# Performance work log

Measured on AMD Instinct MI355X. Metric: run time of the kernel, lower is better.

The kernel has to match this reference:

```python
import jax, jax.numpy as jnp
import numpy as np

N_NODES = 50000
N_EDGES = 800000
D = 64
NEG_SLOPE = 0.01  # torch F.leaky_relu default


def _gin_layer(h, src, dst, eps, W, b, activate):
    # max-aggregate neighbor features: for each dst node, max over incoming src feats
    msg = h[src]  # [E, D] gather
    agg = jax.ops.segment_max(msg, dst, num_segments=N_NODES)  # [N, D]
    # DGL fills nodes with no in-edges with 0 for max reduce
    agg = jnp.where(jnp.isfinite(agg), agg, jnp.zeros((), h.dtype))
    out = ((1.0 + eps) * h + agg) @ W + b
    if activate:
        out = jnp.where(out >= 0, out, NEG_SLOPE * out)
    return out


def setup_inputs() -> dict:
    key = jax.random.key(0)
    ks = jax.random.split(key, 6)
    scale = 1.0 / np.sqrt(D)
    return {
        "n_feat": jax.random.normal(ks[0], (N_NODES, D), dtype=jnp.float32),
        "W0": jax.random.normal(ks[1], (D, D), dtype=jnp.float32) * scale,
        "b0": jnp.zeros((D,), jnp.float32),
        "W1": jax.random.normal(ks[2], (D, D), dtype=jnp.float32) * scale,
        "b1": jnp.zeros((D,), jnp.float32),
        "W2": jax.random.normal(ks[3], (D, D), dtype=jnp.float32) * scale,
        "b2": jnp.zeros((D,), jnp.float32),
        "eps": jnp.zeros((3,), jnp.float32),
        "src": jax.random.randint(ks[4], (N_EDGES,), 0, N_NODES, dtype=jnp.int32),
        "dst": jax.random.randint(ks[5], (N_EDGES,), 0, N_NODES, dtype=jnp.int32),
    }


def reference(n_feat, W0, b0, W1, b1, W2, b2, eps, src, dst):
    h = _gin_layer(n_feat, src, dst, eps[0], W0, b0, activate=True)
    h = _gin_layer(h, src, dst, eps[1], W1, b1, activate=True)
    h = _gin_layer(h, src, dst, eps[2], W2, b2, activate=False)  # last_activate=False
    return h
```

## Files before the change

kernel.cpp:

```cpp
#include <hip/hip_runtime.h>

#define N_NODES 50000
#define N_EDGES 800000
#define D 64
#define CAP 64
#define XLD 72

typedef short short8 __attribute__((ext_vector_type(8)));
typedef float floatx4 __attribute__((ext_vector_type(4)));

__device__ __forceinline__ unsigned short f32_to_bf16(float f) {
    unsigned int u = __float_as_uint(f);
    u += 0x7FFFu + ((u >> 16) & 1u);
    return (unsigned short)(u >> 16);
}
__device__ __forceinline__ float bf16_to_f32(unsigned short h) {
    return __uint_as_float((unsigned int)h << 16);
}

__global__ void __launch_bounds__(256) cvt_kernel(const float* __restrict__ in,
                                                  unsigned short* __restrict__ hb0,
                                                  unsigned short* __restrict__ hb1) {
    int t = blockIdx.x * 256 + threadIdx.x;
    float4 v = ((const float4*)in)[t];
    uint2 o;
    o.x = ((unsigned)f32_to_bf16(v.y) << 16) | f32_to_bf16(v.x);
    o.y = ((unsigned)f32_to_bf16(v.w) << 16) | f32_to_bf16(v.z);
    ((uint2*)hb0)[t] = o;
    if (blockIdx.x == 0) {
        int l = threadIdx.x;
        if (l < 64) hb0[(size_t)N_NODES * 64 + l] = 0xFF80u;
        else if (l < 128) hb1[(size_t)N_NODES * 64 + (l - 64)] = 0xFF80u;
    }
}

__global__ void __launch_bounds__(256) wprep_kernel(const float* __restrict__ W0,
                                                    const float* __restrict__ W1,
                                                    const float* __restrict__ W2,
                                                    unsigned short* __restrict__ wt_all) {
    const float* Ws[3] = {W0, W1, W2};
    const float* W = Ws[blockIdx.x];
    unsigned short* o = wt_all + blockIdx.x * 4096;
    for (int idx = threadIdx.x; idx < 4096; idx += 256) {
        int k = idx >> 6, n = idx & 63;
        o[n * 64 + k] = f32_to_bf16(W[idx]);
    }
}

__global__ void __launch_bounds__(256) fill_kernel(const int* __restrict__ src,
                                                   const int* __restrict__ dst,
                                                   int* __restrict__ cnt,
                                                   int* __restrict__ bucket) {
    int e = blockIdx.x * 256 + threadIdx.x;
    int t = dst[e];
    int slot = atomicAdd(&cnt[t], 1);
    if (slot < CAP) bucket[t * CAP + slot] = src[e] << 6;
}

__global__ void __launch_bounds__(256) pad_kernel(const int* __restrict__ cnt,
                                                  int* __restrict__ bucket) {
    int t = blockIdx.x * 256 + threadIdx.x;
    if (t >= N_NODES) return;
    int c = min(cnt[t], CAP);
    int e4 = (c + 3) & ~3;
    for (int s = c; s < e4; ++s) bucket[t * CAP + s] = N_NODES * 64;
}

__global__ void __launch_bounds__(256) layer_kernel(
        const unsigned short* __restrict__ hin,
        const int* __restrict__ cnt,
        const int* __restrict__ bucket,
        const unsigned short* __restrict__ wt,
        const float* __restrict__ bias,
        const float* __restrict__ eps_arr,
        int layer, int activate, int last,
        unsigned short* __restrict__ out_bf,
        float* __restrict__ out_f32) {
    __shared__ unsigned short xs[16 * XLD];

    const int tid = threadIdx.x;
    const int lane = tid & 63;
    const int wv = tid >> 6;
    const float ev = 1.0f + eps_arr[layer];

    const int r0 = blockIdx.x * 16 + wv * 4;

    int bvec[4], c_true[4], c4[4];
    float self[4];
#pragma unroll
    for (int j = 0; j < 4; ++j) {
        int rr = r0 + j;
        bvec[j] = bucket[rr * CAP + lane];
        c_true[j] = min(cnt[rr], CAP);
        c4[j] = (c_true[j] + 3) & ~3;
        self[j] = bf16_to_f32(hin[rr * 64 + lane]);
    }
    int cmax = max(max(c4[0], c4[1]), max(c4[2], c4[3]));

    float m[4] = {-INFINITY, -INFINITY, -INFINITY, -INFINITY};
    for (int i = 0; i < cmax; i += 4) {
#pragma unroll
        for (int j = 0; j < 4; ++j) {
            if (i < c4[j]) {
                int s0 = __builtin_amdgcn_readlane(bvec[j], i);
                int s1 = __builtin_amdgcn_readlane(bvec[j], i + 1);
                int s2 = __builtin_amdgcn_readlane(bvec[j], i + 2);
                int s3 = __builtin_amdgcn_readlane(bvec[j], i + 3);
                float a0 = bf16_to_f32(hin[s0 + lane]);
                float a1 = bf16_to_f32(hin[s1 + lane]);
                float a2 = bf16_to_f32(hin[s2 + lane]);
                float a3 = bf16_to_f32(hin[s3 + lane]);
                m[j] = fmaxf(m[j], fmaxf(fmaxf(a0, a1), fmaxf(a2, a3)));
            }
        }
    }

#pragma unroll
    for (int j = 0; j < 4; ++j) {
        float agg = (c_true[j] > 0) ? m[j] : 0.0f;
        float x = fmaf(ev, self[j], agg);
        xs[(wv * 4 + j) * XLD + lane] = f32_to_bf16(x);
    }
    __syncthreads();

    const int l15 = lane & 15, hi = lane >> 4;
    const int kc = hi * 8;
    short8 a0 = *(const short8*)&xs[l15 * XLD + kc];
    short8 a1 = *(const short8*)&xs[l15 * XLD + 32 + kc];
    const int ncol = wv * 16 + l15;
    short8 b0 = *(const short8*)&wt[ncol * 64 + kc];
    short8 b1 = *(const short8*)&wt[ncol * 64 + 32 + kc];
    floatx4 acc = {0.f, 0.f, 0.f, 0.f};
    acc = __builtin_amdgcn_mfma_f32_16x16x32_bf16(a0, b0, acc, 0, 0, 0);
    acc = __builtin_amdgcn_mfma_f32_16x16x32_bf16(a1, b1, acc, 0, 0, 0);

    const float bv = bias[ncol];
#pragma unroll
    for (int i = 0; i < 4; ++i) {
        int grow = blockIdx.x * 16 + hi * 4 + i;
        float v = acc[i] + bv;
        if (activate) v = (v >= 0.f) ? v : 0.01f * v;
        if (last) out_f32[(size_t)grow * 64 + ncol] = v;
        else out_bf[(size_t)grow * 64 + ncol] = f32_to_bf16(v);
    }
}

extern "C" void kernel_launch(void* const* d_in, const int* in_sizes, int n_in,
                              void* d_out, int out_size, void* d_ws, size_t ws_size,
                              hipStream_t stream) {
    const float* n_feat = (const float*)d_in[0];
    const float* W0 = (const float*)d_in[1];
    const float* b0 = (const float*)d_in[2];
    const float* W1 = (const float*)d_in[3];
    const float* b1 = (const float*)d_in[4];
    const float* W2 = (const float*)d_in[5];
    const float* b2 = (const float*)d_in[6];
    const float* eps = (const float*)d_in[7];
    const int* src = (const int*)d_in[8];
    const int* dst = (const int*)d_in[9];
    float* out = (float*)d_out;

    const size_t BKT_OFF = 200192;
    const size_t HB0_OFF = BKT_OFF + (size_t)N_NODES * CAP * 4;
    const size_t HB1_OFF = HB0_OFF + (size_t)(N_NODES + 1) * 64 * 2;
    const size_t WT_OFF  = HB1_OFF + (size_t)(N_NODES + 1) * 64 * 2;

    int* cnt = (int*)d_ws;
    int* bucket = (int*)((char*)d_ws + BKT_OFF);
    unsigned short* hb0 = (unsigned short*)((char*)d_ws + HB0_OFF);
    unsigned short* hb1 = (unsigned short*)((char*)d_ws + HB1_OFF);
    unsigned short* wt_all = (unsigned short*)((char*)d_ws + WT_OFF);

    hipMemsetAsync(cnt, 0, (size_t)N_NODES * 4, stream);
    cvt_kernel<<<3125, 256, 0, stream>>>(n_feat, hb0, hb1);
    wprep_kernel<<<3, 256, 0, stream>>>(W0, W1, W2, wt_all);
    fill_kernel<<<N_EDGES / 256, 256, 0, stream>>>(src, dst, cnt, bucket);
    pad_kernel<<<(N_NODES + 255) / 256, 256, 0, stream>>>(cnt, bucket);

    dim3 blk(256), grd(N_NODES / 16);

    layer_kernel<<<grd, blk, 0, stream>>>(hb0, cnt, bucket, wt_all,        b0, eps, 0, 1, 0, hb1, out);
    layer_kernel<<<grd, blk, 0, stream>>>(hb1, cnt, bucket, wt_all + 4096, b1, eps, 1, 1, 0, hb0, out);
    layer_kernel<<<grd, blk, 0, stream>>>(hb0, cnt, bucket, wt_all + 8192, b2, eps, 2, 0, 1, hb1, out);
}
```

Before: 220.6 us.

## Restructure gather to 16-lane groups with 16-bit bucket indices in LDS

The neighbor max-gather is remapped so each 16-lane group handles one destination row and each lane loads four bf16 features (8 bytes) per neighbor, instead of one wave walking all four rows with readlane. Bucket indices are stored as 16-bit values and staged through shared memory, which halves bucket traffic and removes the pad kernel and sentinel row. The conversion and weight-prep kernels are merged into one launch. Storing source indices as ushort truncates node ids above 65535; that holds for 50000 nodes but ties correctness to the node count. Rows within a wave now diverge by per-row edge count.

```diff
diff --git a/kernel.cpp b/kernel.cpp
--- a/kernel.cpp
+++ b/kernel.cpp
@@ -8,131 +8,115 @@
 
 typedef short short8 __attribute__((ext_vector_type(8)));
 typedef float floatx4 __attribute__((ext_vector_type(4)));
+typedef unsigned short ushort_t;
 
-__device__ __forceinline__ unsigned short f32_to_bf16(float f) {
+__device__ __forceinline__ ushort_t f32_to_bf16(float f) {
     unsigned int u = __float_as_uint(f);
     u += 0x7FFFu + ((u >> 16) & 1u);
-    return (unsigned short)(u >> 16);
+    return (ushort_t)(u >> 16);
 }
-__device__ __forceinline__ float bf16_to_f32(unsigned short h) {
-    return __uint_as_float((unsigned int)h << 16);
-}
+__device__ __forceinline__ float bf16lo(unsigned int u) { return __uint_as_float(u << 16); }
+__device__ __forceinline__ float bf16hi(unsigned int u) { return __uint_as_float(u & 0xFFFF0000u); }
 
-__global__ void __launch_bounds__(256) cvt_kernel(const float* __restrict__ in,
-                                                  unsigned short* __restrict__ hb0,
-                                                  unsigned short* __restrict__ hb1) {
+__global__ void __launch_bounds__(256) cvtw_kernel(const float* __restrict__ in,
+                                                   ushort_t* __restrict__ hb0,
+                                                   const float* __restrict__ W0,
+                                                   const float* __restrict__ W1,
+                                                   const float* __restrict__ W2,
+                                                   ushort_t* __restrict__ wt_all) {
     int t = blockIdx.x * 256 + threadIdx.x;
     float4 v = ((const float4*)in)[t];
     uint2 o;
     o.x = ((unsigned)f32_to_bf16(v.y) << 16) | f32_to_bf16(v.x);
     o.y = ((unsigned)f32_to_bf16(v.w) << 16) | f32_to_bf16(v.z);
     ((uint2*)hb0)[t] = o;
-    if (blockIdx.x == 0) {
-        int l = threadIdx.x;
-        if (l < 64) hb0[(size_t)N_NODES * 64 + l] = 0xFF80u;
-        else if (l < 128) hb1[(size_t)N_NODES * 64 + (l - 64)] = 0xFF80u;
-    }
-}
-
-__global__ void __launch_bounds__(256) wprep_kernel(const float* __restrict__ W0,
-                                                    const float* __restrict__ W1,
-                                                    const float* __restrict__ W2,
-                                                    unsigned short* __restrict__ wt_all) {
-    const float* Ws[3] = {W0, W1, W2};
-    const float* W = Ws[blockIdx.x];
-    unsigned short* o = wt_all + blockIdx.x * 4096;
-    for (int idx = threadIdx.x; idx < 4096; idx += 256) {
-        int k = idx >> 6, n = idx & 63;
-        o[n * 64 + k] = f32_to_bf16(W[idx]);
+    if (blockIdx.x < 3) {
+        const float* Ws[3] = {W0, W1, W2};
+        const float* W = Ws[blockIdx.x];
+        ushort_t* ow = wt_all + blockIdx.x * 4096;
+        for (int idx = threadIdx.x; idx < 4096; idx += 256) {
+            int k = idx >> 6, n = idx & 63;
+            ow[n * 64 + k] = f32_to_bf16(W[idx]);
+        }
     }
 }
 
 __global__ void __launch_bounds__(256) fill_kernel(const int* __restrict__ src,
                                                    const int* __restrict__ dst,
                                                    int* __restrict__ cnt,
-                                                   int* __restrict__ bucket) {
+                                                   ushort_t* __restrict__ bucket) {
     int e = blockIdx.x * 256 + threadIdx.x;
     int t = dst[e];
     int slot = atomicAdd(&cnt[t], 1);
-    if (slot < CAP) bucket[t * CAP + slot] = src[e] << 6;
-}
-
-__global__ void __launch_bounds__(256) pad_kernel(const int* __restrict__ cnt,
-                                                  int* __restrict__ bucket) {
-    int t = blockIdx.x * 256 + threadIdx.x;
-    if (t >= N_NODES) return;
-    int c = min(cnt[t], CAP);
-    int e4 = (c + 3) & ~3;
-    for (int s = c; s < e4; ++s) bucket[t * CAP + s] = N_NODES * 64;
+    if (slot < CAP) bucket[t * CAP + slot] = (ushort_t)src[e];
 }
 
 __global__ void __launch_bounds__(256) layer_kernel(
-        const unsigned short* __restrict__ hin,
+        const ushort_t* __restrict__ hin,
         const int* __restrict__ cnt,
-        const int* __restrict__ bucket,
-        const unsigned short* __restrict__ wt,
+        const ushort_t* __restrict__ bucket,
+        const ushort_t* __restrict__ wt,
         const float* __restrict__ bias,
         const float* __restrict__ eps_arr,
         int layer, int activate, int last,
-        unsigned short* __restrict__ out_bf,
+        ushort_t* __restrict__ out_bf,
         float* __restrict__ out_f32) {
-    __shared__ unsigned short xs[16 * XLD];
+    __shared__ ushort_t bk[16 * CAP];
+    __shared__ ushort_t xs[16 * XLD];
 
     const int tid = threadIdx.x;
     const int lane = tid & 63;
     const int wv = tid >> 6;
+    const int grp = lane >> 4;
+    const int fo = (lane & 15) * 4;
     const float ev = 1.0f + eps_arr[layer];
 
     const int r0 = blockIdx.x * 16 + wv * 4;
 
-    int bvec[4], c_true[4], c4[4];
-    float self[4];
 #pragma unroll
-    for (int j = 0; j < 4; ++j) {
-        int rr = r0 + j;
-        bvec[j] = bucket[rr * CAP + lane];
-        c_true[j] = min(cnt[rr], CAP);
-        c4[j] = (c_true[j] + 3) & ~3;
-        self[j] = bf16_to_f32(hin[rr * 64 + lane]);
-    }
-    int cmax = max(max(c4[0], c4[1]), max(c4[2], c4[3]));
+    for (int j = 0; j < 4; ++j)
+        bk[(wv * 4 + j) * CAP + lane] = bucket[(r0 + j) * CAP + lane];
 
-    float m[4] = {-INFINITY, -INFINITY, -INFINITY, -INFINITY};
-    for (int i = 0; i < cmax; i += 4) {
-#pragma unroll
-        for (int j = 0; j < 4; ++j) {
-            if (i < c4[j]) {
-                int s0 = __builtin_amdgcn_readlane(bvec[j], i);
-                int s1 = __builtin_amdgcn_readlane(bvec[j], i + 1);
-                int s2 = __builtin_amdgcn_readlane(bvec[j], i + 2);
-                int s3 = __builtin_amdgcn_readlane(bvec[j], i + 3);
-                float a0 = bf16_to_f32(hin[s0 + lane]);
-                float a1 = bf16_to_f32(hin[s1 + lane]);
-                float a2 = bf16_to_f32(hin[s2 + lane]);
-                float a3 = bf16_to_f32(hin[s3 + lane]);
-                m[j] = fmaxf(m[j], fmaxf(fmaxf(a0, a1), fmaxf(a2, a3)));
-            }
+    const int rr = r0 + grp;
+    int cg = min(cnt[rr], CAP);
+    int c0 = __builtin_amdgcn_readlane(cg, 0);
+    int c1 = __builtin_amdgcn_readlane(cg, 16);
+    int c2 = __builtin_amdgcn_readlane(cg, 32);
+    int c3 = __builtin_amdgcn_readlane(cg, 48);
+    int cmax = max(max(c0, c1), max(c2, c3));
+
+    const uint2 sv = *(const uint2*)&hin[rr * 64 + fo];
+
+    float m0 = -INFINITY, m1 = -INFINITY, m2 = -INFINITY, m3 = -INFINITY;
+    const ushort_t* bkrow = &bk[(wv * 4 + grp) * CAP];
+    for (int i = 0; i < cmax; ++i) {
+        if (i < cg) {
+            int s = bkrow[i];
+            const uint2 u = *(const uint2*)&hin[s * 64 + fo];
+            m0 = fmaxf(m0, bf16lo(u.x)); m1 = fmaxf(m1, bf16hi(u.x));
+            m2 = fmaxf(m2, bf16lo(u.y)); m3 = fmaxf(m3, bf16hi(u.y));
         }
     }
-
-#pragma unroll
-    for (int j = 0; j < 4; ++j) {
-        float agg = (c_true[j] > 0) ? m[j] : 0.0f;
-        float x = fmaf(ev, self[j], agg);
-        xs[(wv * 4 + j) * XLD + lane] = f32_to_bf16(x);
-    }
+    float a0 = (cg > 0) ? m0 : 0.f, a1 = (cg > 0) ? m1 : 0.f;
+    float a2 = (cg > 0) ? m2 : 0.f, a3 = (cg > 0) ? m3 : 0.f;
+    float x0 = fmaf(ev, bf16lo(sv.x), a0), x1 = fmaf(ev, bf16hi(sv.x), a1);
+    float x2 = fmaf(ev, bf16lo(sv.y), a2), x3 = fmaf(ev, bf16hi(sv.y), a3);
+    uint2 w;
+    w.x = ((unsigned)f32_to_bf16(x1) << 16) | f32_to_bf16(x0);
+    w.y = ((unsigned)f32_to_bf16(x3) << 16) | f32_to_bf16(x2);
+    *(uint2*)&xs[(wv * 4 + grp) * XLD + fo] = w;
     __syncthreads();
 
     const int l15 = lane & 15, hi = lane >> 4;
     const int kc = hi * 8;
-    short8 a0 = *(const short8*)&xs[l15 * XLD + kc];
-    short8 a1 = *(const short8*)&xs[l15 * XLD + 32 + kc];
+    short8 fa0 = *(const short8*)&xs[l15 * XLD + kc];
+    short8 fa1 = *(const short8*)&xs[l15 * XLD + 32 + kc];
     const int ncol = wv * 16 + l15;
-    short8 b0 = *(const short8*)&wt[ncol * 64 + kc];
-    short8 b1 = *(const short8*)&wt[ncol * 64 + 32 + kc];
+    short8 fb0 = *(const short8*)&wt[ncol * 64 + kc];
+    short8 fb1 = *(const short8*)&wt[ncol * 64 + 32 + kc];
     floatx4 acc = {0.f, 0.f, 0.f, 0.f};
-    acc = __builtin_amdgcn_mfma_f32_16x16x32_bf16(a0, b0, acc, 0, 0, 0);
-    acc = __builtin_amdgcn_mfma_f32_16x16x32_bf16(a1, b1, acc, 0, 0, 0);
+    acc = __builtin_amdgcn_mfma_f32_16x16x32_bf16(fa0, fb0, acc, 0, 0, 0);
+    acc = __builtin_amdgcn_mfma_f32_16x16x32_bf16(fa1, fb1, acc, 0, 0, 0);
 
     const float bv = bias[ncol];
 #pragma unroll
@@ -161,25 +145,23 @@
     float* out = (float*)d_out;
 
     const size_t BKT_OFF = 200192;
-    const size_t HB0_OFF = BKT_OFF + (size_t)N_NODES * CAP * 4;
-    const size_t HB1_OFF = HB0_OFF + (size_t)(N_NODES + 1) * 64 * 2;
-    const size_t WT_OFF  = HB1_OFF + (size_t)(N_NODES + 1) * 64 * 2;
+    const size_t HB0_OFF = BKT_OFF + (size_t)N_NODES * CAP * 2;
+    const size_t HB1_OFF = HB0_OFF + (size_t)N_NODES * 64 * 2;
+    const size_t WT_OFF  = HB1_OFF + (size_t)N_NODES * 64 * 2;
 
     int* cnt = (int*)d_ws;
-    int* bucket = (int*)((char*)d_ws + BKT_OFF);
-    unsigned short* hb0 = (unsigned short*)((char*)d_ws + HB0_OFF);
-    unsigned short* hb1 = (unsigned short*)((char*)d_ws + HB1_OFF);
-    unsigned short* wt_all = (unsigned short*)((char*)d_ws + WT_OFF);
+    ushort_t* bucket = (ushort_t*)((char*)d_ws + BKT_OFF);
+    ushort_t* hb0 = (ushort_t*)((char*)d_ws + HB0_OFF);
+    ushort_t* hb1 = (ushort_t*)((char*)d_ws + HB1_OFF);
+    ushort_t* wt_all = (ushort_t*)((char*)d_ws + WT_OFF);
 
     hipMemsetAsync(cnt, 0, (size_t)N_NODES * 4, stream);
-    cvt_kernel<<<3125, 256, 0, stream>>>(n_feat, hb0, hb1);
-    wprep_kernel<<<3, 256, 0, stream>>>(W0, W1, W2, wt_all);
+    cvtw_kernel<<<3125, 256, 0, stream>>>(n_feat, hb0, W0, W1, W2, wt_all);
     fill_kernel<<<N_EDGES / 256, 256, 0, stream>>>(src, dst, cnt, bucket);
-    pad_kernel<<<(N_NODES + 255) / 256, 256, 0, stream>>>(cnt, bucket);
 
-    dim3 blk(256), grd(N_NODES / 16);
+    dim3 blk(256), grd(N_NODES / 16 + 1);
 
-    layer_kernel<<<grd, blk, 0, stream>>>(hb0, cnt, bucket, wt_all,        b0, eps, 0, 1, 0, hb1, out);
-    layer_kernel<<<grd, blk, 0, stream>>>(hb1, cnt, bucket, wt_all + 4096, b1, eps, 1, 1, 0, hb0, out);
-    layer_kernel<<<grd, blk, 0, stream>>>(hb0, cnt, bucket, wt_all + 8192, b2, eps, 2, 0, 1, hb1, out);
+    layer_kernel<<<3125, blk, 0, stream>>>(hb0, cnt, bucket, wt_all,        b0, eps, 0, 1, 0, hb1, out);
+    layer_kernel<<<3125, blk, 0, stream>>>(hb1, cnt, bucket, wt_all + 4096, b1, eps, 1, 1, 0, hb0, out);
+    layer_kernel<<<3125, blk, 0, stream>>>(hb0, cnt, bucket, wt_all + 8192, b2, eps, 2, 0, 1, hb1, out);
 }
```

After: 212.6 us. 1.04x faster.
